# Optimization experiments

Hardware: AMD Instinct MI355X
Metric: run time of the kernel (lower is better)

The kernel has to match this reference:

```python
import jax, jax.numpy as jnp
import numpy as np
from jax import lax

H = 8  # hardcoded in the module (node indices 0..7)


def setup_inputs() -> dict:
    k = jax.random.key(0)
    k1, k2, k3, k4, k5 = jax.random.split(k, 5)
    B, S, D = 1024, 7, 4096  # seq MUST be 7 (Conv1d uses it as channels)
    query = jax.random.normal(k1, (B, S, D), jnp.float32)
    key = jax.random.normal(k2, (B, S, D), jnp.float32)
    value = jax.random.normal(k3, (B, S, D), jnp.float32)
    conv_w = jax.random.normal(k4, (7, 7, 3), jnp.float32) * 0.05  # Conv1d(7,7,3) OIW
    conv_b = jnp.zeros((7,), jnp.float32)
    w_out = jax.random.normal(k5, (D, D), jnp.float32) * 0.02  # linears[-1].weight
    b_out = jnp.zeros((D,), jnp.float32)
    return {"query": query, "key": key, "value": value,
            "conv_w": conv_w, "conv_b": conv_b, "w_out": w_out, "b_out": b_out}


def reference(query, key, value, conv_w, conv_b, w_out, b_out):
    B, S, D = query.shape
    dk = D // H
    # split q/k/v into H chunks of d_k along last dim -> [B, H, S, dk]
    split = lambda t: jnp.moveaxis(t.reshape(B, S, H, dk), 2, 1)
    q, kk, v = split(query), split(key), split(value)
    # node_i = cat(key_i, value_i, query_i) -> [B, H, S, 3dk]
    node = jnp.concatenate([kk, v, q], axis=-1)
    # neighbor sums along the head axis: s0=n0+n1, s_i=n_{i-1}+n_i+n_{i+1}, s7=n6+n7
    npad = jnp.pad(node, ((0, 0), (1, 1), (0, 0), (0, 0)))
    s = npad[:, :-2] + npad[:, 1:-1] + npad[:, 2:]  # [B, H, S, 3dk]
    # shared Conv1d(7,7,3,stride=1,pad=1) over the 3dk axis; channels = S = 7
    x = s.reshape(B * H, S, 3 * dk)
    x = lax.conv_general_dilated(x, conv_w, window_strides=(1,), padding=((1, 1),),
                                 dimension_numbers=("NCW", "OIW", "NCW"))
    x = x + conv_b[None, :, None]
    x = x.reshape(B, H, S, 3 * dk)
    # re-split: [0]=k', [1]=v', [2]=q'; attention(q', k', v')
    k2, v2, q2 = x[..., :dk], x[..., dk:2 * dk], x[..., 2 * dk:]
    scores = jnp.einsum("bhqd,bhkd->bhqk", q2, k2) * (1.0 / (dk ** 0.5))
    p = jax.nn.softmax(scores, axis=-1)
    atn = jnp.einsum("bhqk,bhkd->bhqd", p, v2)  # [B, H, S, dk]
    out = jnp.moveaxis(atn, 1, 2).reshape(B, S, D)  # concat heads
    return out @ w_out.T + b_out  # linears[-1]
```

## Files before the change

### kernel.cpp

```cpp
#include <hip/hip_runtime.h>
#include <hip/hip_bf16.h>

#define Hh 8
#define Bb 1024
#define Ss 7
#define Dd 4096
#define DK 512
#define W3 1536
#define COLS 1544
#define Mrows (Bb*Ss)

typedef float  f32x4  __attribute__((ext_vector_type(4)));
typedef short  bf16x8 __attribute__((ext_vector_type(8)));

static __device__ __forceinline__ unsigned short f2bf(float f) {
  union { float f; unsigned int u; } v; v.f = f;
  unsigned int u = v.u;
  u += 0x7FFFu + ((u >> 16) & 1u);
  return (unsigned short)(u >> 16);
}

static __device__ __forceinline__ void gload_lds16(const void* g, void* l) {
  __builtin_amdgcn_global_load_lds(
      (const __attribute__((address_space(1))) unsigned int*)g,
      (__attribute__((address_space(3))) unsigned int*)l,
      16, 0, 0);
}

__global__ __launch_bounds__(256) void attn_kernel(
    const float* __restrict__ qg, const float* __restrict__ kg, const float* __restrict__ vg,
    const float* __restrict__ cw, const float* __restrict__ cb,
    unsigned short* __restrict__ Abf)
{
  __shared__ float sbuf[Ss][COLS];
  __shared__ float cw_s[147];
  __shared__ float cb_s[7];
  __shared__ float scores_s[49];
  __shared__ float pmat[Ss][Ss];

  const int t  = threadIdx.x;
  const int bh = blockIdx.x;
  const int b  = bh >> 3, h = bh & 7;

  if (t < 147) cw_s[t] = cw[t];
  if (t < 7)   cb_s[t] = cb[t];
  if (t < 7) { sbuf[t][3] = 0.f; sbuf[t][4 + W3] = 0.f; }

  #pragma unroll
  for (int j = 0; j < 11; ++j) {
    int slot = j * 256 + t;
    if (slot < 2688) {
      int i   = slot / 384;
      int rem = slot - i * 384;
      int r   = rem >> 7;
      int c   = rem & 127;
      const float* src = (r == 0) ? kg : (r == 1) ? vg : qg;
      long base = (long)(b * Ss + i) * Dd + h * DK + c * 4;
      float4 s = *(const float4*)(src + base);
      if (h > 0) { float4 a = *(const float4*)(src + base - DK); s.x+=a.x; s.y+=a.y; s.z+=a.z; s.w+=a.w; }
      if (h < 7) { float4 a = *(const float4*)(src + base + DK); s.x+=a.x; s.y+=a.y; s.z+=a.z; s.w+=a.w; }
      *(float4*)&sbuf[i][4 + r * DK + c * 4] = s;
    }
  }
  __syncthreads();

  float xo[42];
  #pragma unroll
  for (int j = 0; j < 42; ++j) {
    int slot = j * 256 + t;
    int o = slot / W3;
    int w = slot - o * W3;
    float acc = cb_s[o];
    #pragma unroll
    for (int i = 0; i < 7; ++i) {
      const float* sp = &sbuf[i][3 + w];
      const float* wp = &cw_s[(o * 7 + i) * 3];
      acc += wp[0] * sp[0] + wp[1] * sp[1] + wp[2] * sp[2];
    }
    xo[j] = acc;
  }
  __syncthreads();
  #pragma unroll
  for (int j = 0; j < 42; ++j) {
    int slot = j * 256 + t;
    int o = slot / W3;
    int w = slot - o * W3;
    sbuf[o][4 + w] = xo[j];
  }
  __syncthreads();

  const int wave = t >> 6, lane = t & 63;
  for (int p = wave; p < 49; p += 4) {
    int qq = p / 7, kk = p % 7;
    const float4 a0 = *(const float4*)&sbuf[qq][4 + 2 * DK + lane * 8];
    const float4 a1 = *(const float4*)&sbuf[qq][4 + 2 * DK + lane * 8 + 4];
    const float4 b0 = *(const float4*)&sbuf[kk][4 + lane * 8];
    const float4 b1 = *(const float4*)&sbuf[kk][4 + lane * 8 + 4];
    float part = a0.x*b0.x + a0.y*b0.y + a0.z*b0.z + a0.w*b0.w
               + a1.x*b1.x + a1.y*b1.y + a1.z*b1.z + a1.w*b1.w;
    #pragma unroll
    for (int off = 32; off; off >>= 1) part += __shfl_xor(part, off);
    if (lane == 0) scores_s[p] = part * 0.044194173824159216f;
  }
  __syncthreads();

  if (t < 7) {
    float row[7], m = -1e30f;
    #pragma unroll
    for (int kk = 0; kk < 7; ++kk) { row[kk] = scores_s[t * 7 + kk]; m = fmaxf(m, row[kk]); }
    float s = 0.f;
    #pragma unroll
    for (int kk = 0; kk < 7; ++kk) { row[kk] = expf(row[kk] - m); s += row[kk]; }
    float inv = 1.0f / s;
    #pragma unroll
    for (int kk = 0; kk < 7; ++kk) pmat[t][kk] = row[kk] * inv;
  }
  __syncthreads();

  #pragma unroll
  for (int qq = 0; qq < 7; ++qq) {
    int d = t * 2;
    float a0 = 0.f, a1 = 0.f;
    #pragma unroll
    for (int kk = 0; kk < 7; ++kk) {
      float pk = pmat[qq][kk];
      a0 += pk * sbuf[kk][4 + DK + d];
      a1 += pk * sbuf[kk][4 + DK + d + 1];
    }
    unsigned int packed = ((unsigned int)f2bf(a1) << 16) | (unsigned int)f2bf(a0);
    *(unsigned int*)&Abf[(long)(b * Ss + qq) * Dd + h * DK + d] = packed;
  }
}

__global__ __launch_bounds__(256) void castw(const float* __restrict__ w, unsigned short* __restrict__ o)
{
  const int total = (Dd * Dd) / 4;
  for (int s = blockIdx.x * 256 + threadIdx.x; s < total; s += gridDim.x * 256) {
    float4 f = *(const float4*)(w + (long)s * 4);
    ushort4 u;
    u.x = f2bf(f.x); u.y = f2bf(f.y); u.z = f2bf(f.z); u.w = f2bf(f.w);
    *(ushort4*)(o + (long)s * 4) = u;
  }
}

#define BM 128
#define BN 128
#define BK 32

__global__ __launch_bounds__(256) void gemm_bt(
    const unsigned short* __restrict__ A, const unsigned short* __restrict__ Bt,
    const float* __restrict__ bias, float* __restrict__ C)
{
  __shared__ unsigned short As[BM * BK];
  __shared__ unsigned short Bs[BN * BK];

  const int t    = threadIdx.x;
  const int m0   = blockIdx.y * BM;
  const int n0   = blockIdx.x * BN;
  const int wave = t >> 6, lane = t & 63;
  const int wm   = (wave >> 1) * 64, wn = (wave & 1) * 64;
  const int lr   = lane & 15, lk = (lane >> 4) * 8;

  const int srow = t >> 2;
  const int scol = (t & 3) * 8;

  f32x4 acc[4][4] = {};

  for (int kt = 0; kt < Dd / BK; ++kt) {
    const int k0 = kt * BK;
    #pragma unroll
    for (int j = 0; j < 2; ++j) {
      const int row = j * 64 + srow;
      gload_lds16(A  + (long)(m0 + row) * Dd + k0 + scol, &As[row * BK + scol]);
      gload_lds16(Bt + (long)(n0 + row) * Dd + k0 + scol, &Bs[row * BK + scol]);
    }
    __syncthreads();

    bf16x8 af[4], bfr[4];
    #pragma unroll
    for (int mi = 0; mi < 4; ++mi) af[mi]  = *(const bf16x8*)&As[(wm + mi * 16 + lr) * BK + lk];
    #pragma unroll
    for (int ni = 0; ni < 4; ++ni) bfr[ni] = *(const bf16x8*)&Bs[(wn + ni * 16 + lr) * BK + lk];
    #pragma unroll
    for (int mi = 0; mi < 4; ++mi)
      #pragma unroll
      for (int ni = 0; ni < 4; ++ni)
        acc[mi][ni] = __builtin_amdgcn_mfma_f32_16x16x32_bf16(af[mi], bfr[ni], acc[mi][ni], 0, 0, 0);
    __syncthreads();
  }

  #pragma unroll
  for (int ni = 0; ni < 4; ++ni) {
    const int col = n0 + wn + ni * 16 + lr;
    const float bi = bias[col];
    #pragma unroll
    for (int mi = 0; mi < 4; ++mi) {
      const int rbase = m0 + wm + mi * 16 + (lane >> 4) * 4;
      #pragma unroll
      for (int r = 0; r < 4; ++r)
        C[(long)(rbase + r) * Dd + col] = acc[mi][ni][r] + bi;
    }
  }
}

extern "C" void kernel_launch(void* const* d_in, const int* in_sizes, int n_in,
                              void* d_out, int out_size, void* d_ws, size_t ws_size,
                              hipStream_t stream) {
  const float* qg = (const float*)d_in[0];
  const float* kg = (const float*)d_in[1];
  const float* vg = (const float*)d_in[2];
  const float* cw = (const float*)d_in[3];
  const float* cb = (const float*)d_in[4];
  const float* wo = (const float*)d_in[5];
  const float* bo = (const float*)d_in[6];
  float* out = (float*)d_out;

  unsigned short* Abf = (unsigned short*)d_ws;
  unsigned short* Wbf = Abf + (size_t)Mrows * Dd;

  hipLaunchKernelGGL(castw,       dim3(2048),   dim3(256), 0, stream, wo, Wbf);
  hipLaunchKernelGGL(attn_kernel, dim3(Bb * Hh), dim3(256), 0, stream, qg, kg, vg, cw, cb, Abf);
  hipLaunchKernelGGL(gemm_bt,     dim3(Dd / BN, Mrows / BM), dim3(256), 0, stream, Abf, Wbf, bo, out);
}
```

Measured before the change: 995.5 us.

## Exploit conv channel-segment separability to shrink attention LDS and remap GEMM tiles

The attention kernel now treats the k, v and q segments of the 1536-wide conv row as separate 512-wide buffers with one-element halos pulled from the neighbouring segment. This cuts LDS from about 43KB to about 29KB so more blocks fit per CU (launch bounds 5). V is convolved in registers after the scores are computed, and each thread computes two adjacent outputs for all 7 channels, which reuses loaded inputs. The GEMM gets a 1D grid with an XCD-aware tile swizzle for better L2 locality. Risks are the added register pressure and the extra scalar halo loads.

Result: slower. 1.019 ms (+2.3%).

```diff
diff --git a/kernel.cpp b/kernel.cpp
--- a/kernel.cpp
+++ b/kernel.cpp
@@ -6,11 +6,11 @@
 #define Ss 7
 #define Dd 4096
 #define DK 512
-#define W3 1536
-#define COLS 1544
 #define Mrows (Bb*Ss)
+#define RS 520
 
 typedef float  f32x4  __attribute__((ext_vector_type(4)));
+typedef float  f32x2  __attribute__((ext_vector_type(2)));
 typedef short  bf16x8 __attribute__((ext_vector_type(8)));
 
 static __device__ __forceinline__ unsigned short f2bf(float f) {
@@ -27,77 +27,89 @@
       16, 0, 0);
 }
 
-__global__ __launch_bounds__(256) void attn_kernel(
+static __device__ __forceinline__ float sum3s(const float* __restrict__ src, int b, int i, int h, int c) {
+  long base = (long)(b * Ss + i) * Dd + h * DK + c;
+  float v = src[base];
+  if (h > 0) v += src[base - DK];
+  if (h < 7) v += src[base + DK];
+  return v;
+}
+
+__global__ __launch_bounds__(256, 5) void attn_kernel(
     const float* __restrict__ qg, const float* __restrict__ kg, const float* __restrict__ vg,
     const float* __restrict__ cw, const float* __restrict__ cb,
     unsigned short* __restrict__ Abf)
 {
-  __shared__ float sbuf[Ss][COLS];
-  __shared__ float cw_s[147];
+  __shared__ float bufA[Ss][RS];
+  __shared__ float bufB[Ss][RS];
+  __shared__ float cw4[49][4];
   __shared__ float cb_s[7];
   __shared__ float scores_s[49];
-  __shared__ float pmat[Ss][Ss];
-
-  const int t  = threadIdx.x;
-  const int bh = blockIdx.x;
-  const int b  = bh >> 3, h = bh & 7;
-
-  if (t < 147) cw_s[t] = cw[t];
-  if (t < 7)   cb_s[t] = cb[t];
-  if (t < 7) { sbuf[t][3] = 0.f; sbuf[t][4 + W3] = 0.f; }
-
-  #pragma unroll
-  for (int j = 0; j < 11; ++j) {
+  __shared__ float pmat[7][7];
+
+  const int t    = threadIdx.x;
+  const int bh   = blockIdx.x;
+  const int b    = bh >> 3, h = bh & 7;
+  const int lane = t & 63, wave = t >> 6;
+
+  if (t < 147) { int oi = t / 3; cw4[oi][t - oi * 3] = cw[t]; }
+  if (t < 7) {
+    cb_s[t] = cb[t];
+    bufA[t][3]   = 0.f;
+    bufA[t][516] = sum3s(vg, b, t, h, 0);
+    bufB[t][3]   = sum3s(vg, b, t, h, 511);
+    bufB[t][516] = 0.f;
+  }
+
+  #pragma unroll
+  for (int j = 0; j < 7; ++j) {
     int slot = j * 256 + t;
-    if (slot < 2688) {
-      int i   = slot / 384;
-      int rem = slot - i * 384;
-      int r   = rem >> 7;
-      int c   = rem & 127;
-      const float* src = (r == 0) ? kg : (r == 1) ? vg : qg;
-      long base = (long)(b * Ss + i) * Dd + h * DK + c * 4;
-      float4 s = *(const float4*)(src + base);
-      if (h > 0) { float4 a = *(const float4*)(src + base - DK); s.x+=a.x; s.y+=a.y; s.z+=a.z; s.w+=a.w; }
-      if (h < 7) { float4 a = *(const float4*)(src + base + DK); s.x+=a.x; s.y+=a.y; s.z+=a.z; s.w+=a.w; }
-      *(float4*)&sbuf[i][4 + r * DK + c * 4] = s;
-    }
-  }
-  __syncthreads();
-
-  float xo[42];
-  #pragma unroll
-  for (int j = 0; j < 42; ++j) {
-    int slot = j * 256 + t;
-    int o = slot / W3;
-    int w = slot - o * W3;
-    float acc = cb_s[o];
-    #pragma unroll
-    for (int i = 0; i < 7; ++i) {
-      const float* sp = &sbuf[i][3 + w];
-      const float* wp = &cw_s[(o * 7 + i) * 3];
-      acc += wp[0] * sp[0] + wp[1] * sp[1] + wp[2] * sp[2];
-    }
-    xo[j] = acc;
-  }
-  __syncthreads();
-  #pragma unroll
-  for (int j = 0; j < 42; ++j) {
-    int slot = j * 256 + t;
-    int o = slot / W3;
-    int w = slot - o * W3;
-    sbuf[o][4 + w] = xo[j];
-  }
-  __syncthreads();
-
-  const int wave = t >> 6, lane = t & 63;
+    int isK  = slot < 896;
+    int s2   = isK ? slot : slot - 896;
+    int i    = s2 >> 7, c4 = (s2 & 127) << 2;
+    const float* src = isK ? kg : qg;
+    float* dst = isK ? &bufA[i][4 + c4] : &bufB[i][4 + c4];
+    long base = (long)(b * Ss + i) * Dd + h * DK + c4;
+    float4 v = *(const float4*)(src + base);
+    if (h > 0) { float4 a = *(const float4*)(src + base - DK); v.x+=a.x; v.y+=a.y; v.z+=a.z; v.w+=a.w; }
+    if (h < 7) { float4 a = *(const float4*)(src + base + DK); v.x+=a.x; v.y+=a.y; v.z+=a.z; v.w+=a.w; }
+    *(float4*)dst = v;
+  }
+  __syncthreads();
+
+  const int w2 = 2 * t;
+  float ok0[7], ok1[7], oq0[7], oq1[7];
+  #pragma unroll
+  for (int o = 0; o < 7; ++o) { float c0 = cb_s[o]; ok0[o]=c0; ok1[o]=c0; oq0[o]=c0; oq1[o]=c0; }
+  #pragma unroll
+  for (int i = 0; i < 7; ++i) {
+    float a0 = bufA[i][3+w2], a1 = bufA[i][4+w2], a2 = bufA[i][5+w2], a3 = bufA[i][6+w2];
+    float q0 = bufB[i][3+w2], q1 = bufB[i][4+w2], q2 = bufB[i][5+w2], q3 = bufB[i][6+w2];
+    #pragma unroll
+    for (int o = 0; o < 7; ++o) {
+      f32x4 wv = *(const f32x4*)&cw4[o*7+i][0];
+      ok0[o] += wv[0]*a0 + wv[1]*a1 + wv[2]*a2;
+      ok1[o] += wv[0]*a1 + wv[1]*a2 + wv[2]*a3;
+      oq0[o] += wv[0]*q0 + wv[1]*q1 + wv[2]*q2;
+      oq1[o] += wv[0]*q1 + wv[1]*q2 + wv[2]*q3;
+    }
+  }
+  __syncthreads();
+  #pragma unroll
+  for (int o = 0; o < 7; ++o) {
+    *(f32x2*)&bufA[o][4 + w2] = (f32x2){ok0[o], ok1[o]};
+    *(f32x2*)&bufB[o][4 + w2] = (f32x2){oq0[o], oq1[o]};
+  }
+  __syncthreads();
+
   for (int p = wave; p < 49; p += 4) {
-    int qq = p / 7, kk = p % 7;
-    const float4 a0 = *(const float4*)&sbuf[qq][4 + 2 * DK + lane * 8];
-    const float4 a1 = *(const float4*)&sbuf[qq][4 + 2 * DK + lane * 8 + 4];
-    const float4 b0 = *(const float4*)&sbuf[kk][4 + lane * 8];
-    const float4 b1 = *(const float4*)&sbuf[kk][4 + lane * 8 + 4];
-    float part = a0.x*b0.x + a0.y*b0.y + a0.z*b0.z + a0.w*b0.w
-               + a1.x*b1.x + a1.y*b1.y + a1.z*b1.z + a1.w*b1.w;
+    int qq = p / 7, kk = p - qq * 7;
+    f32x4 x0 = *(const f32x4*)&bufB[qq][4 + lane * 4];
+    f32x4 x1 = *(const f32x4*)&bufB[qq][4 + 256 + lane * 4];
+    f32x4 y0 = *(const f32x4*)&bufA[kk][4 + lane * 4];
+    f32x4 y1 = *(const f32x4*)&bufA[kk][4 + 256 + lane * 4];
+    float part = x0[0]*y0[0] + x0[1]*y0[1] + x0[2]*y0[2] + x0[3]*y0[3]
+               + x1[0]*y1[0] + x1[1]*y1[1] + x1[2]*y1[2] + x1[3]*y1[3];
     #pragma unroll
     for (int off = 32; off; off >>= 1) part += __shfl_xor(part, off);
     if (lane == 0) scores_s[p] = part * 0.044194173824159216f;
@@ -107,28 +119,50 @@
   if (t < 7) {
     float row[7], m = -1e30f;
     #pragma unroll
-    for (int kk = 0; kk < 7; ++kk) { row[kk] = scores_s[t * 7 + kk]; m = fmaxf(m, row[kk]); }
+    for (int k = 0; k < 7; ++k) { row[k] = scores_s[t * 7 + k]; m = fmaxf(m, row[k]); }
     float s = 0.f;
     #pragma unroll
-    for (int kk = 0; kk < 7; ++kk) { row[kk] = expf(row[kk] - m); s += row[kk]; }
+    for (int k = 0; k < 7; ++k) { row[k] = __expf(row[k] - m); s += row[k]; }
     float inv = 1.0f / s;
     #pragma unroll
-    for (int kk = 0; kk < 7; ++kk) pmat[t][kk] = row[kk] * inv;
-  }
-  __syncthreads();
-
+    for (int k = 0; k < 7; ++k) pmat[t][k] = row[k] * inv;
+    bufB[t][3]   = sum3s(kg, b, t, h, 511);
+    bufB[t][516] = sum3s(qg, b, t, h, 0);
+  }
+  #pragma unroll
+  for (int j = 0; j < 4; ++j) {
+    int slot = j * 256 + t;
+    if (slot < 896) {
+      int i = slot >> 7, c4 = (slot & 127) << 2;
+      long base = (long)(b * Ss + i) * Dd + h * DK + c4;
+      float4 v = *(const float4*)(vg + base);
+      if (h > 0) { float4 a = *(const float4*)(vg + base - DK); v.x+=a.x; v.y+=a.y; v.z+=a.z; v.w+=a.w; }
+      if (h < 7) { float4 a = *(const float4*)(vg + base + DK); v.x+=a.x; v.y+=a.y; v.z+=a.z; v.w+=a.w; }
+      *(float4*)&bufB[i][4 + c4] = v;
+    }
+  }
+  __syncthreads();
+
+  float ov0[7], ov1[7];
+  #pragma unroll
+  for (int o = 0; o < 7; ++o) { float c0 = cb_s[o]; ov0[o] = c0; ov1[o] = c0; }
+  #pragma unroll
+  for (int i = 0; i < 7; ++i) {
+    float v0 = bufB[i][3+w2], v1 = bufB[i][4+w2], v2 = bufB[i][5+w2], v3 = bufB[i][6+w2];
+    #pragma unroll
+    for (int o = 0; o < 7; ++o) {
+      f32x4 wv = *(const f32x4*)&cw4[o*7+i][0];
+      ov0[o] += wv[0]*v0 + wv[1]*v1 + wv[2]*v2;
+      ov1[o] += wv[0]*v1 + wv[1]*v2 + wv[2]*v3;
+    }
+  }
   #pragma unroll
   for (int qq = 0; qq < 7; ++qq) {
-    int d = t * 2;
     float a0 = 0.f, a1 = 0.f;
     #pragma unroll
-    for (int kk = 0; kk < 7; ++kk) {
-      float pk = pmat[qq][kk];
-      a0 += pk * sbuf[kk][4 + DK + d];
-      a1 += pk * sbuf[kk][4 + DK + d + 1];
-    }
+    for (int k = 0; k < 7; ++k) { float pk = pmat[qq][k]; a0 += pk * ov0[k]; a1 += pk * ov1[k]; }
     unsigned int packed = ((unsigned int)f2bf(a1) << 16) | (unsigned int)f2bf(a0);
-    *(unsigned int*)&Abf[(long)(b * Ss + qq) * Dd + h * DK + d] = packed;
+    *(unsigned int*)&Abf[(long)(b * Ss + qq) * Dd + h * DK + w2] = packed;
   }
 }
 
@@ -146,6 +180,8 @@
 #define BM 128
 #define BN 128
 #define BK 32
+#define NTILES (Dd / BN)
+#define MTILES (Mrows / BM)
 
 __global__ __launch_bounds__(256) void gemm_bt(
     const unsigned short* __restrict__ A, const unsigned short* __restrict__ Bt,
@@ -154,9 +190,12 @@
   __shared__ unsigned short As[BM * BK];
   __shared__ unsigned short Bs[BN * BK];
 
+  const int wg = blockIdx.x;
+  const int sw = (wg & 7) * (NTILES * MTILES / 8) + (wg >> 3);
+  const int m0 = (sw >> 5) * BM;
+  const int n0 = (sw & 31) * BN;
+
   const int t    = threadIdx.x;
-  const int m0   = blockIdx.y * BM;
-  const int n0   = blockIdx.x * BN;
   const int wave = t >> 6, lane = t & 63;
   const int wm   = (wave >> 1) * 64, wn = (wave & 1) * 64;
   const int lr   = lane & 15, lk = (lane >> 4) * 8;
@@ -218,7 +257,7 @@
   unsigned short* Abf = (unsigned short*)d_ws;
   unsigned short* Wbf = Abf + (size_t)Mrows * Dd;
 
-  hipLaunchKernelGGL(castw,       dim3(2048),   dim3(256), 0, stream, wo, Wbf);
+  hipLaunchKernelGGL(castw,       dim3(2048),    dim3(256), 0, stream, wo, Wbf);
   hipLaunchKernelGGL(attn_kernel, dim3(Bb * Hh), dim3(256), 0, stream, qg, kg, vg, cw, cb, Abf);
-  hipLaunchKernelGGL(gemm_bt,     dim3(Dd / BN, Mrows / BM), dim3(256), 0, stream, Abf, Wbf, bo, out);
-}
+  hipLaunchKernelGGL(gemm_bt,     dim3(NTILES * MTILES), dim3(256), 0, stream, Abf, Wbf, bo, out);
+}
```
